# Kernel tuning notes

Hardware: AMD Instinct MI355X
Metric: run time of the kernel (lower is better)

## Reference

```python
import jax, jax.numpy as jnp
import numpy as np
from jax import lax

NUM_CLASSES = 2
MAX_DET = 300
SCORE_THR = 0.001
IOU_THR = 0.7
EPS = 1e-7


def _probiou_pairwise(b):
    # b: [M,5] = (cx, cy, w, h, angle). Gaussian-based rotated-box IoU (ProbIoU).
    cx, cy, w, h, t = (b[:, i] for i in range(5))
    ct, st = jnp.cos(t), jnp.sin(t)
    w2, h2 = w * w / 12.0, h * h / 12.0
    a = w2 * ct * ct + h2 * st * st
    bb = w2 * st * st + h2 * ct * ct
    c = (w2 - h2) * ct * st
    x1, y1, a1, b1, c1 = cx[:, None], cy[:, None], a[:, None], bb[:, None], c[:, None]
    x2, y2, a2, b2, c2 = cx[None, :], cy[None, :], a[None, :], bb[None, :], c[None, :]
    denom = (a1 + a2) * (b1 + b2) - (c1 + c2) ** 2 + EPS
    t1 = 0.25 * ((a1 + a2) * (y1 - y2) ** 2 + (b1 + b2) * (x1 - x2) ** 2) / denom
    t2 = 0.5 * ((c1 + c2) * (x2 - x1) * (y1 - y2)) / denom
    det1 = jnp.maximum(a1 * b1 - c1 * c1, 0.0)
    det2 = jnp.maximum(a2 * b2 - c2 * c2, 0.0)
    t3 = 0.5 * jnp.log(denom / (4.0 * jnp.sqrt(det1 * det2) + EPS) + EPS)
    bd = jnp.clip(t1 + t2 + t3, EPS, 100.0)
    hd = jnp.sqrt(1.0 - jnp.exp(-bd) + EPS)
    return 1.0 - hd


def _nms_single(boxes5, scores):
    # boxes5: [N,5], scores: [N,C] -> class-aware greedy rotated NMS
    N, C = scores.shape
    M = N * C
    cand_boxes = jnp.broadcast_to(boxes5[:, None, :], (N, C, 5)).reshape(M, 5)
    cand_scores = scores.reshape(M)
    cand_labels = jnp.broadcast_to(jnp.arange(C, dtype=jnp.int32)[None, :], (N, C)).reshape(M)
    order = jnp.argsort(-cand_scores)
    b, s, l = cand_boxes[order], cand_scores[order], cand_labels[order]
    iou = _probiou_pairwise(b)                          # [M,M]
    same = l[:, None] == l[None, :]
    sup = (iou > IOU_THR) & same
    idx = jnp.arange(M)
    valid = s > SCORE_THR

    def body(i, keep):
        row = sup[i] & (idx > i) & keep[i]
        return keep & ~row

    keep = lax.fori_loop(0, M, body, valid)
    sel = jnp.where(keep, s, -1.0)
    top = jnp.argsort(-sel)[:MAX_DET]
    ok = sel[top] > 0.0
    out_boxes = jnp.where(ok[:, None], b[top], 0.0)     # [MAX_DET,5]
    out_scores = jnp.where(ok, s[top], 0.0)             # [MAX_DET]
    out_labels = jnp.where(ok, l[top], 0)               # [MAX_DET] int32
    n_valid = jnp.minimum(jnp.sum(keep), MAX_DET).astype(jnp.int32)
    return out_boxes, out_scores, out_labels, n_valid


def _forward(x, conv_w, conv_b, bbox_w, bbox_b, cls_w, cls_b, ang_w, ang_b):
    B = x.shape[0]
    f = lax.conv_general_dilated(x, conv_w, (1, 1), 'SAME',
                                 dimension_numbers=('NCHW', 'OIHW', 'NCHW'))
    f = jax.nn.relu(f + conv_b[None, :, None, None])
    f = lax.reduce_window(f, -jnp.inf, lax.max, (1, 1, 2, 2), (1, 1, 2, 2), 'VALID')
    Hp, Wp = f.shape[2], f.shape[3]
    hw = Hp * Wp
    # 1x1-conv heads (materialized like the original), then spatial mean
    boxes = (jnp.einsum('bchw,oc->bohw', f, bbox_w) + bbox_b[None, :, None, None]
             ).reshape(B, MAX_DET, 4, hw).mean(-1)
    logits = (jnp.einsum('bchw,oc->bohw', f, cls_w) + cls_b[None, :, None, None]
              ).reshape(B, MAX_DET, NUM_CLASSES, hw).mean(-1)
    scores = jax.nn.softmax(logits, axis=2)
    angles = (jnp.einsum('bchw,oc->bohw', f, ang_w) + ang_b[None, :, None, None]
              ).reshape(B, MAX_DET, 1, hw).mean(-1)
    boxes5 = jnp.concatenate([boxes, angles], axis=-1)  # [B,300,5]
    return jax.vmap(_nms_single)(boxes5, scores)


def setup_inputs() -> dict:
    key = jax.random.key(0)
    ks = jax.random.split(key, 10)
    B, H, W = 4, 256, 256
    s = 0.1
    return {
        'x': jax.random.normal(ks[0], (B, 3, H, W), jnp.float32),
        'conv_w': jax.random.normal(ks[1], (16, 3, 3, 3), jnp.float32) * s,
        'conv_b': jax.random.normal(ks[2], (16,), jnp.float32) * s,
        'bbox_w': jax.random.normal(ks[3], (4 * MAX_DET, 16), jnp.float32) * s,
        'bbox_b': jax.random.normal(ks[4], (4 * MAX_DET,), jnp.float32) * s,
        'cls_w': jax.random.normal(ks[5], (NUM_CLASSES * MAX_DET, 16), jnp.float32) * s,
        'cls_b': jax.random.normal(ks[6], (NUM_CLASSES * MAX_DET,), jnp.float32) * s,
        'ang_w': jax.random.normal(ks[7], (MAX_DET, 16), jnp.float32) * s,
        'ang_b': jax.random.normal(ks[8], (MAX_DET,), jnp.float32) * s,
    }


def reference(x, conv_w, conv_b, bbox_w, bbox_b, cls_w, cls_b, ang_w, ang_b):
    return _forward(x, conv_w, conv_b, bbox_w, bbox_b, cls_w, cls_b, ang_w, ang_b)
```

## Files before the change

kernel.cpp:

```cpp
#include <hip/hip_runtime.h>
#include <hip/hip_bf16.h>

#define MAX_DET 300
#define NCAND 600
#define NPAD 640
#define SCORE_THR 1e-3f
#define IOU_THR 0.7f
#define EPSF 1e-7f

typedef float float4u __attribute__((ext_vector_type(4), aligned(4)));


static __device__ inline unsigned long long readlane64(unsigned long long v, int l) {
  unsigned int lo = (unsigned int)v;
  unsigned int hi = (unsigned int)(v >> 32);
  unsigned int slo = (unsigned int)__builtin_amdgcn_readlane((int)lo, l);
  unsigned int shi = (unsigned int)__builtin_amdgcn_readlane((int)hi, l);
  return ((unsigned long long)shi << 32) | (unsigned long long)slo;
}

__global__ __launch_bounds__(256) void k_conv_pool(
    const float* __restrict__ x, const float* __restrict__ cw,
    const float* __restrict__ cb, float* __restrict__ partial) {
  const int blk = blockIdx.x;
  const int chunk = blk & 7;
  const int oc = (blk >> 3) & 15;
  const int b = blk >> 7;
  const int tid = threadIdx.x;

  float w[27];
#pragma unroll
  for (int i = 0; i < 27; ++i) w[i] = cw[oc * 27 + i];
  const float bias = cb[oc];
  const float* xb = x + b * 3 * 65536;

  const int strip = chunk * 256 + tid;
  const int py = strip >> 4;
  const int x0 = (strip & 15) * 8;

  float cc0[8], cc1[8], cc2[8], cc3[8];
#pragma unroll
  for (int i = 0; i < 8; ++i) { cc0[i] = 0.f; cc1[i] = 0.f; cc2[i] = 0.f; cc3[i] = 0.f; }

#pragma unroll
  for (int ic = 0; ic < 3; ++ic) {
    const float* xc = xb + ic * 65536;
    const float* wc = w + ic * 9;
#pragma unroll
    for (int r = 0; r < 4; ++r) {
      const int y = 2 * py - 1 + r;
      if (y < 0 || y > 255) continue;
      const float* xr = xc + y * 256;
      float buf[20];
#pragma unroll
      for (int k = 0; k < 5; ++k) {
        const int c0 = 2 * x0 - 1 + 4 * k;
        if (c0 >= 0 && c0 + 3 <= 255) {
          const float4u v = *reinterpret_cast<const float4u*>(xr + c0);
          buf[4 * k + 0] = v.x; buf[4 * k + 1] = v.y;
          buf[4 * k + 2] = v.z; buf[4 * k + 3] = v.w;
        } else {
#pragma unroll
          for (int j = 0; j < 4; ++j) {
            const int c = c0 + j;
            buf[4 * k + j] = (c >= 0 && c <= 255) ? xr[c] : 0.f;
          }
        }
      }
#pragma unroll
      for (int i = 0; i < 8; ++i) {
        const float b0 = buf[2 * i], b1 = buf[2 * i + 1],
                    b2 = buf[2 * i + 2], b3 = buf[2 * i + 3];
        if (r <= 2) {
          const float w0 = wc[r * 3], w1 = wc[r * 3 + 1], w2 = wc[r * 3 + 2];
          cc0[i] += b0 * w0 + b1 * w1 + b2 * w2;
          cc1[i] += b1 * w0 + b2 * w1 + b3 * w2;
        }
        if (r >= 1) {
          const float w0 = wc[(r - 1) * 3], w1 = wc[(r - 1) * 3 + 1],
                      w2 = wc[(r - 1) * 3 + 2];
          cc2[i] += b0 * w0 + b1 * w1 + b2 * w2;
          cc3[i] += b1 * w0 + b2 * w1 + b3 * w2;
        }
      }
    }
  }

  float acc = 0.f;
#pragma unroll
  for (int i = 0; i < 8; ++i) {
    const float m = fmaxf(fmaxf(cc0[i], cc1[i]), fmaxf(cc2[i], cc3[i]));
    acc += fmaxf(m + bias, 0.f);
  }

  __shared__ float red[256];
  red[tid] = acc;
  __syncthreads();
  for (int s = 128; s > 0; s >>= 1) {
    if (tid < s) red[tid] += red[tid + s];
    __syncthreads();
  }
  if (tid == 0) partial[blk] = red[0];
}

__global__ __launch_bounds__(256) void k_prep(
    const float* __restrict__ partial,
    const float* __restrict__ bw, const float* __restrict__ bb,
    const float* __restrict__ cwm, const float* __restrict__ cbb,
    const float* __restrict__ aw, const float* __restrict__ ab,
    float* __restrict__ boxes5, float* __restrict__ sparams,
    int* __restrict__ order_g) {
  const int b = blockIdx.x;
  const int tid = threadIdx.x;
  const int wid = tid >> 6, lane = tid & 63;

  __shared__ float fm[16];
  __shared__ float sc[NPAD];
  __shared__ float sbox[MAX_DET * 5];
  __shared__ int order[NCAND];

  if (tid < 16) {
    float s = 0.f;
    for (int k = 0; k < 8; ++k) s += partial[(b * 16 + tid) * 8 + k];
    fm[tid] = s * (1.0f / 16384.0f);
  }
  for (int m = NCAND + tid; m < NPAD; m += 256) sc[m] = -1e30f;
  __syncthreads();

  float f[16];
#pragma unroll
  for (int k = 0; k < 16; ++k) f[k] = fm[k];

  for (int det = tid; det < MAX_DET; det += 256) {
    float out5[5];
#pragma unroll
    for (int j = 0; j < 4; ++j) {
      const int o = det * 4 + j;
      float acc = bb[o];
#pragma unroll
      for (int k = 0; k < 16; ++k) acc += bw[o * 16 + k] * f[k];
      out5[j] = acc;
    }
    {
      float acc = ab[det];
#pragma unroll
      for (int k = 0; k < 16; ++k) acc += aw[det * 16 + k] * f[k];
      out5[4] = acc;
    }
    float l0, l1;
    {
      const int o = det * 2;
      float a0 = cbb[o], a1 = cbb[o + 1];
#pragma unroll
      for (int k = 0; k < 16; ++k) {
        a0 += cwm[o * 16 + k] * f[k];
        a1 += cwm[(o + 1) * 16 + k] * f[k];
      }
      l0 = a0; l1 = a1;
    }
    const float mx = fmaxf(l0, l1);
    const float e0 = expf(l0 - mx), e1 = expf(l1 - mx);
    const float inv = 1.f / (e0 + e1);

#pragma unroll
    for (int j = 0; j < 5; ++j) {
      sbox[det * 5 + j] = out5[j];
      boxes5[(b * MAX_DET + det) * 5 + j] = out5[j];
    }
    sc[det * 2 + 0] = e0 * inv;
    sc[det * 2 + 1] = e1 * inv;
  }
  __syncthreads();

  float sreg[10];
#pragma unroll
  for (int k = 0; k < 10; ++k) sreg[k] = sc[k * 64 + lane];

#pragma unroll
  for (int w = 0; w < 10; ++w) {
#pragma unroll
    for (int t = 0; t < 16; ++t) {
      const int i = w * 64 + wid + 4 * t;
      if (i < NCAND) {
        float si;
        switch (w) {
          case 0: si = __shfl(sreg[0], i & 63); break;
          case 1: si = __shfl(sreg[1], i & 63); break;
          case 2: si = __shfl(sreg[2], i & 63); break;
          case 3: si = __shfl(sreg[3], i & 63); break;
          case 4: si = __shfl(sreg[4], i & 63); break;
          case 5: si = __shfl(sreg[5], i & 63); break;
          case 6: si = __shfl(sreg[6], i & 63); break;
          case 7: si = __shfl(sreg[7], i & 63); break;
          case 8: si = __shfl(sreg[8], i & 63); break;
          default: si = __shfl(sreg[9], i & 63); break;
        }
        int r = 0;
#pragma unroll
        for (int k = 0; k < 10; ++k) {
          const int j = k * 64 + lane;
          const bool c = (sreg[k] > si) || (sreg[k] == si && j < i);
          r += (int)__popcll(__ballot(c));
        }
        if (lane == 0) order[r] = i;
      }
    }
  }
  __syncthreads();

  float* P = sparams + b * 7 * NPAD;
  for (int r = tid; r < NCAND; r += 256) {
    const int i = order[r];
    order_g[b * NPAD + r] = i;
    const float* bp = sbox + (i >> 1) * 5;
    const float cx = bp[0], cy = bp[1], w = bp[2], h = bp[3], t = bp[4];
    const float ct = cosf(t), st = sinf(t);
    const float w2 = w * w * (1.f / 12.f), h2 = h * h * (1.f / 12.f);
    const float a = w2 * ct * ct + h2 * st * st;
    const float bb2 = w2 * st * st + h2 * ct * ct;
    const float c = (w2 - h2) * ct * st;
    P[0 * NPAD + r] = cx;
    P[1 * NPAD + r] = cy;
    P[2 * NPAD + r] = a;
    P[3 * NPAD + r] = bb2;
    P[4 * NPAD + r] = c;
    P[5 * NPAD + r] = fmaxf(a * bb2 - c * c, 0.f);
    P[6 * NPAD + r] = sc[i];
  }
}

__global__ __launch_bounds__(256) void k_mask(
    const float* __restrict__ sparams, const int* __restrict__ order_g,
    unsigned long long* __restrict__ mask) {
  const int wid = threadIdx.x >> 6, lane = threadIdx.x & 63;
  const int g = blockIdx.x * 4 + wid;
  const int b = g / NCAND, i = g % NCAND;

  const float* P = sparams + b * 7 * NPAD;
  const int* og = order_g + b * NPAD;
  const float x1 = P[i], y1 = P[NPAD + i], a1 = P[2 * NPAD + i],
              b1 = P[3 * NPAD + i], c1 = P[4 * NPAD + i], d1 = P[5 * NPAD + i];
  const int li = og[i] & 1;

#pragma unroll
  for (int w = 0; w < 10; ++w) {
    const int j = w * 64 + lane;
    const int jc = j < NCAND ? j : NCAND - 1;
    const float x2 = P[jc], y2 = P[NPAD + jc], a2 = P[2 * NPAD + jc],
                b2 = P[3 * NPAD + jc], c2 = P[4 * NPAD + jc],
                d2 = P[5 * NPAD + jc];
    const float as = a1 + a2, bs = b1 + b2, cs = c1 + c2;
    const float dxx = x2 - x1, dyy = y1 - y2;
    const float denom = as * bs - cs * cs + EPSF;
    const float rden = 1.f / denom;
    const float t1v = 0.25f * (as * dyy * dyy + bs * dxx * dxx) * rden;
    const float t2v = 0.5f * (cs * dxx * dyy) * rden;
    const float t3v = 0.5f * logf(denom / (4.f * sqrtf(d1 * d2) + EPSF) + EPSF);
    float bd = t1v + t2v + t3v;
    bd = fminf(fmaxf(bd, EPSF), 100.f);
    const float hd = sqrtf(1.f - expf(-bd) + EPSF);
    const bool cond = (j > i) && (j < NCAND) && ((og[jc] & 1) == li) &&
                      ((1.f - hd) > IOU_THR);
    const unsigned long long mw = __ballot(cond);
    if (lane == 0) mask[(b * NCAND + i) * 10 + w] = mw;
  }
}

__global__ __launch_bounds__(256) void k_scan(
    const float* __restrict__ boxes5, const float* __restrict__ sparams,
    const int* __restrict__ order_g, const unsigned long long* __restrict__ mask,
    float* __restrict__ out) {
  const int b = blockIdx.x;
  const int tid = threadIdx.x;
  const int wid = tid >> 6, lane = tid & 63;

  __shared__ unsigned long long m[NCAND * 10];
  __shared__ float ssc[NCAND];
  __shared__ unsigned long long keepw[10];
  __shared__ unsigned long long validbm[10];
  __shared__ unsigned long long nzbm[10];

  const unsigned long long* mg = mask + b * NCAND * 10;
  for (int k = tid; k < NCAND * 10; k += 256) m[k] = mg[k];
  const float* P = sparams + b * 7 * NPAD;
  for (int k = tid; k < NCAND; k += 256) ssc[k] = P[6 * NPAD + k];
  __syncthreads();

#pragma unroll
  for (int it = 0; it < 3; ++it) {
    const int g = wid + 4 * it;
    if (g < 10) {
      const int r = g * 64 + lane;
      bool valid = false;
      unsigned long long nzr = 0ULL;
      if (r < NCAND) {
        valid = ssc[r] > SCORE_THR;
        for (int k = 0; k < 10; ++k) nzr |= m[r * 10 + k];
      }
      const unsigned long long vb = __ballot(valid);
      const unsigned long long nb = __ballot(nzr != 0ULL);
      if (lane == 0) { validbm[g] = vb; nzbm[g] = nb; }
    }
  }
  __syncthreads();

  if (tid < 64) {
    unsigned long long keep = (lane < 10) ? validbm[lane] : 0ULL;
    const unsigned long long nzv = (lane < 10) ? nzbm[lane] : 0ULL;
#pragma unroll
    for (int w = 0; w < 10; ++w) {
      unsigned long long nzs = readlane64(nzv, w);
      unsigned long long ks = readlane64(keep, w);
      while (nzs) {
        const int bit = __builtin_ctzll(nzs);
        nzs &= nzs - 1ULL;
        if ((ks >> bit) & 1ULL) {
          const int i = w * 64 + bit;
          unsigned long long row = 0ULL;
          if (lane < 10) row = m[i * 10 + lane];
          keep &= ~row;
          ks &= ~readlane64(row, w);
        }
      }
    }
    if (lane < 10) keepw[lane] = keep;
  }
  __syncthreads();

  for (int k = tid; k < MAX_DET * 5; k += 256) out[b * MAX_DET * 5 + k] = 0.f;
  for (int k = tid; k < MAX_DET; k += 256) {
    out[6000 + b * MAX_DET + k] = 0.f;
    out[7200 + b * MAX_DET + k] = 0.f;
  }
  __syncthreads();

  const int* og = order_g + b * NPAD;
  for (int r = tid; r < NCAND; r += 256) {
    const int w = r >> 6, bitp = r & 63;
    if ((keepw[w] >> bitp) & 1ULL) {
      int pos = 0;
      for (int ww = 0; ww < w; ++ww) pos += __popcll(keepw[ww]);
      pos += __popcll(keepw[w] & ((1ULL << bitp) - 1ULL));
      if (pos < MAX_DET) {
        const int i = og[r];
        const float* bp = boxes5 + (b * MAX_DET + (i >> 1)) * 5;
        float* ob = out + (b * MAX_DET + pos) * 5;
        ob[0] = bp[0]; ob[1] = bp[1]; ob[2] = bp[2]; ob[3] = bp[3]; ob[4] = bp[4];
        out[6000 + b * MAX_DET + pos] = ssc[r];
        out[7200 + b * MAX_DET + pos] = (float)(i & 1);
      }
    }
  }
  if (tid == 0) {
    int total = 0;
    for (int ww = 0; ww < 10; ++ww) total += __popcll(keepw[ww]);
    if (total > MAX_DET) total = MAX_DET;
    out[8400 + b] = (float)total;
  }
}

extern "C" void kernel_launch(void* const* d_in, const int* in_sizes, int n_in,
                              void* d_out, int out_size, void* d_ws, size_t ws_size,
                              hipStream_t stream) {
  const float* x      = (const float*)d_in[0];
  const float* conv_w = (const float*)d_in[1];
  const float* conv_b = (const float*)d_in[2];
  const float* bbox_w = (const float*)d_in[3];
  const float* bbox_b = (const float*)d_in[4];
  const float* cls_w  = (const float*)d_in[5];
  const float* cls_b  = (const float*)d_in[6];
  const float* ang_w  = (const float*)d_in[7];
  const float* ang_b  = (const float*)d_in[8];
  float* out = (float*)d_out;
  float* ws = (float*)d_ws;

  float* partial = ws;
  float* boxes5  = ws + 1024;
  float* sparams = ws + 8720;
  int*   order_g = (int*)(ws + 26640);
  unsigned long long* mask = (unsigned long long*)(ws + 29200);

  k_conv_pool<<<512, 256, 0, stream>>>(x, conv_w, conv_b, partial);
  k_prep<<<4, 256, 0, stream>>>(partial, bbox_w, bbox_b, cls_w, cls_b,
                                ang_w, ang_b, boxes5, sparams, order_g);
  k_mask<<<600, 256, 0, stream>>>(sparams, order_g, mask);
  k_scan<<<4, 256, 0, stream>>>(boxes5, sparams, order_g, mask, out);
}
```

Before: 66.21 us.

## Fuse mask and scan kernels via last-block atomic counter; simplify prep

Merges the IoU mask kernel and the greedy NMS scan kernel into one launch. An atomic per-image counter elects the last finishing block, which then runs the scan, so one kernel launch and its inter-kernel gap go away. A hipMemsetAsync is added to reset the counters, and the last block per image adds a serial tail after its own mask work. The prep kernel also splits the linear heads into per-output loops with vectorized weight loads, and the rank computation is simplified to read scores from LDS instead of the switch-based shuffles.

```diff
diff --git a/kernel.cpp b/kernel.cpp
--- a/kernel.cpp
+++ b/kernel.cpp
@@ -131,44 +131,49 @@
 #pragma unroll
   for (int k = 0; k < 16; ++k) f[k] = fm[k];
 
-  for (int det = tid; det < MAX_DET; det += 256) {
-    float out5[5];
-#pragma unroll
-    for (int j = 0; j < 4; ++j) {
-      const int o = det * 4 + j;
-      float acc = bb[o];
-#pragma unroll
-      for (int k = 0; k < 16; ++k) acc += bw[o * 16 + k] * f[k];
-      out5[j] = acc;
-    }
-    {
-      float acc = ab[det];
-#pragma unroll
-      for (int k = 0; k < 16; ++k) acc += aw[det * 16 + k] * f[k];
-      out5[4] = acc;
-    }
-    float l0, l1;
-    {
-      const int o = det * 2;
-      float a0 = cbb[o], a1 = cbb[o + 1];
-#pragma unroll
-      for (int k = 0; k < 16; ++k) {
-        a0 += cwm[o * 16 + k] * f[k];
-        a1 += cwm[(o + 1) * 16 + k] * f[k];
-      }
-      l0 = a0; l1 = a1;
-    }
-    const float mx = fmaxf(l0, l1);
-    const float e0 = expf(l0 - mx), e1 = expf(l1 - mx);
+  for (int o = tid; o < 4 * MAX_DET; o += 256) {
+    const float4u* wp = reinterpret_cast<const float4u*>(bw + o * 16);
+    const float4u v0 = wp[0], v1 = wp[1], v2 = wp[2], v3 = wp[3];
+    float wrow[16] = {v0.x, v0.y, v0.z, v0.w, v1.x, v1.y, v1.z, v1.w,
+                      v2.x, v2.y, v2.z, v2.w, v3.x, v3.y, v3.z, v3.w};
+    float acc = bb[o];
+#pragma unroll
+    for (int k = 0; k < 16; ++k) acc += wrow[k] * f[k];
+    const int d = o >> 2, j = o & 3;
+    sbox[d * 5 + j] = acc;
+    boxes5[(b * MAX_DET + d) * 5 + j] = acc;
+  }
+  for (int o = tid; o < MAX_DET; o += 256) {
+    const float4u* wp = reinterpret_cast<const float4u*>(aw + o * 16);
+    const float4u v0 = wp[0], v1 = wp[1], v2 = wp[2], v3 = wp[3];
+    float wrow[16] = {v0.x, v0.y, v0.z, v0.w, v1.x, v1.y, v1.z, v1.w,
+                      v2.x, v2.y, v2.z, v2.w, v3.x, v3.y, v3.z, v3.w};
+    float acc = ab[o];
+#pragma unroll
+    for (int k = 0; k < 16; ++k) acc += wrow[k] * f[k];
+    sbox[o * 5 + 4] = acc;
+    boxes5[(b * MAX_DET + o) * 5 + 4] = acc;
+  }
+  for (int p = tid; p < MAX_DET; p += 256) {
+    const float4u* wp0 = reinterpret_cast<const float4u*>(cwm + (2 * p) * 16);
+    const float4u* wp1 = reinterpret_cast<const float4u*>(cwm + (2 * p + 1) * 16);
+    const float4u u0 = wp0[0], u1 = wp0[1], u2 = wp0[2], u3 = wp0[3];
+    const float4u t0 = wp1[0], t1 = wp1[1], t2 = wp1[2], t3 = wp1[3];
+    float w0r[16] = {u0.x, u0.y, u0.z, u0.w, u1.x, u1.y, u1.z, u1.w,
+                     u2.x, u2.y, u2.z, u2.w, u3.x, u3.y, u3.z, u3.w};
+    float w1r[16] = {t0.x, t0.y, t0.z, t0.w, t1.x, t1.y, t1.z, t1.w,
+                     t2.x, t2.y, t2.z, t2.w, t3.x, t3.y, t3.z, t3.w};
+    float a0 = cbb[2 * p], a1 = cbb[2 * p + 1];
+#pragma unroll
+    for (int k = 0; k < 16; ++k) {
+      a0 += w0r[k] * f[k];
+      a1 += w1r[k] * f[k];
+    }
+    const float mx = fmaxf(a0, a1);
+    const float e0 = expf(a0 - mx), e1 = expf(a1 - mx);
     const float inv = 1.f / (e0 + e1);
-
-#pragma unroll
-    for (int j = 0; j < 5; ++j) {
-      sbox[det * 5 + j] = out5[j];
-      boxes5[(b * MAX_DET + det) * 5 + j] = out5[j];
-    }
-    sc[det * 2 + 0] = e0 * inv;
-    sc[det * 2 + 1] = e1 * inv;
+    sc[p * 2 + 0] = e0 * inv;
+    sc[p * 2 + 1] = e1 * inv;
   }
   __syncthreads();
 
@@ -176,35 +181,18 @@
 #pragma unroll
   for (int k = 0; k < 10; ++k) sreg[k] = sc[k * 64 + lane];
 
-#pragma unroll
-  for (int w = 0; w < 10; ++w) {
-#pragma unroll
-    for (int t = 0; t < 16; ++t) {
-      const int i = w * 64 + wid + 4 * t;
-      if (i < NCAND) {
-        float si;
-        switch (w) {
-          case 0: si = __shfl(sreg[0], i & 63); break;
-          case 1: si = __shfl(sreg[1], i & 63); break;
-          case 2: si = __shfl(sreg[2], i & 63); break;
-          case 3: si = __shfl(sreg[3], i & 63); break;
-          case 4: si = __shfl(sreg[4], i & 63); break;
-          case 5: si = __shfl(sreg[5], i & 63); break;
-          case 6: si = __shfl(sreg[6], i & 63); break;
-          case 7: si = __shfl(sreg[7], i & 63); break;
-          case 8: si = __shfl(sreg[8], i & 63); break;
-          default: si = __shfl(sreg[9], i & 63); break;
-        }
-        int r = 0;
-#pragma unroll
-        for (int k = 0; k < 10; ++k) {
-          const int j = k * 64 + lane;
-          const bool c = (sreg[k] > si) || (sreg[k] == si && j < i);
-          r += (int)__popcll(__ballot(c));
-        }
-        if (lane == 0) order[r] = i;
-      }
-    }
+#pragma unroll 4
+  for (int t = 0; t < 150; ++t) {
+    const int i = t * 4 + wid;
+    const float si = sc[i];
+    int r = 0;
+#pragma unroll
+    for (int k = 0; k < 10; ++k) {
+      const int j = k * 64 + lane;
+      const bool c = (sreg[k] > si) || (sreg[k] == si && j < i);
+      r += (int)__popcll(__ballot(c));
+    }
+    if (lane == 0) order[r] = i;
   }
   __syncthreads();
 
@@ -229,50 +217,56 @@
   }
 }
 
-__global__ __launch_bounds__(256) void k_mask(
-    const float* __restrict__ sparams, const int* __restrict__ order_g,
-    unsigned long long* __restrict__ mask) {
-  const int wid = threadIdx.x >> 6, lane = threadIdx.x & 63;
-  const int g = blockIdx.x * 4 + wid;
-  const int b = g / NCAND, i = g % NCAND;
+__global__ __launch_bounds__(256) void k_masknms(
+    const float* __restrict__ boxes5, const float* __restrict__ sparams,
+    const int* __restrict__ order_g, unsigned long long* __restrict__ mask,
+    int* __restrict__ cnt, float* __restrict__ out) {
+  const int blk = blockIdx.x;
+  const int b = blk / 150;
+  const int tid = threadIdx.x;
+  const int wid = tid >> 6, lane = tid & 63;
+  const int i = (blk % 150) * 4 + wid;
 
   const float* P = sparams + b * 7 * NPAD;
   const int* og = order_g + b * NPAD;
-  const float x1 = P[i], y1 = P[NPAD + i], a1 = P[2 * NPAD + i],
-              b1 = P[3 * NPAD + i], c1 = P[4 * NPAD + i], d1 = P[5 * NPAD + i];
-  const int li = og[i] & 1;
-
-#pragma unroll
-  for (int w = 0; w < 10; ++w) {
-    const int j = w * 64 + lane;
-    const int jc = j < NCAND ? j : NCAND - 1;
-    const float x2 = P[jc], y2 = P[NPAD + jc], a2 = P[2 * NPAD + jc],
-                b2 = P[3 * NPAD + jc], c2 = P[4 * NPAD + jc],
-                d2 = P[5 * NPAD + jc];
-    const float as = a1 + a2, bs = b1 + b2, cs = c1 + c2;
-    const float dxx = x2 - x1, dyy = y1 - y2;
-    const float denom = as * bs - cs * cs + EPSF;
-    const float rden = 1.f / denom;
-    const float t1v = 0.25f * (as * dyy * dyy + bs * dxx * dxx) * rden;
-    const float t2v = 0.5f * (cs * dxx * dyy) * rden;
-    const float t3v = 0.5f * logf(denom / (4.f * sqrtf(d1 * d2) + EPSF) + EPSF);
-    float bd = t1v + t2v + t3v;
-    bd = fminf(fmaxf(bd, EPSF), 100.f);
-    const float hd = sqrtf(1.f - expf(-bd) + EPSF);
-    const bool cond = (j > i) && (j < NCAND) && ((og[jc] & 1) == li) &&
-                      ((1.f - hd) > IOU_THR);
-    const unsigned long long mw = __ballot(cond);
-    if (lane == 0) mask[(b * NCAND + i) * 10 + w] = mw;
-  }
-}
-
-__global__ __launch_bounds__(256) void k_scan(
-    const float* __restrict__ boxes5, const float* __restrict__ sparams,
-    const int* __restrict__ order_g, const unsigned long long* __restrict__ mask,
-    float* __restrict__ out) {
-  const int b = blockIdx.x;
-  const int tid = threadIdx.x;
-  const int wid = tid >> 6, lane = tid & 63;
+  {
+    const float x1 = P[i], y1 = P[NPAD + i], a1 = P[2 * NPAD + i],
+                b1 = P[3 * NPAD + i], c1 = P[4 * NPAD + i], d1 = P[5 * NPAD + i];
+    const int li = og[i] & 1;
+#pragma unroll
+    for (int w = 0; w < 10; ++w) {
+      const int j = w * 64 + lane;
+      const int jc = j < NCAND ? j : NCAND - 1;
+      const float x2 = P[jc], y2 = P[NPAD + jc], a2 = P[2 * NPAD + jc],
+                  b2 = P[3 * NPAD + jc], c2 = P[4 * NPAD + jc],
+                  d2 = P[5 * NPAD + jc];
+      const float as = a1 + a2, bs = b1 + b2, cs = c1 + c2;
+      const float dxx = x2 - x1, dyy = y1 - y2;
+      const float denom = as * bs - cs * cs + EPSF;
+      const float rden = 1.f / denom;
+      const float t1v = 0.25f * (as * dyy * dyy + bs * dxx * dxx) * rden;
+      const float t2v = 0.5f * (cs * dxx * dyy) * rden;
+      const float t3v = 0.5f * logf(denom / (4.f * sqrtf(d1 * d2) + EPSF) + EPSF);
+      float bd = t1v + t2v + t3v;
+      bd = fminf(fmaxf(bd, EPSF), 100.f);
+      const float hd = sqrtf(1.f - expf(-bd) + EPSF);
+      const bool cond = (j > i) && (j < NCAND) && ((og[jc] & 1) == li) &&
+                        ((1.f - hd) > IOU_THR);
+      const unsigned long long mw = __ballot(cond);
+      if (lane == 0) mask[(b * NCAND + i) * 10 + w] = mw;
+    }
+  }
+
+  __shared__ int lastflag;
+  __threadfence();
+  __syncthreads();
+  if (tid == 0) {
+    const int old = atomicAdd(&cnt[b], 1);
+    lastflag = (old == 149);
+  }
+  __syncthreads();
+  if (!lastflag) return;
+  __threadfence();
 
   __shared__ unsigned long long m[NCAND * 10];
   __shared__ float ssc[NCAND];
@@ -282,7 +276,6 @@
 
   const unsigned long long* mg = mask + b * NCAND * 10;
   for (int k = tid; k < NCAND * 10; k += 256) m[k] = mg[k];
-  const float* P = sparams + b * 7 * NPAD;
   for (int k = tid; k < NCAND; k += 256) ssc[k] = P[6 * NPAD + k];
   __syncthreads();
 
@@ -315,9 +308,9 @@
         const int bit = __builtin_ctzll(nzs);
         nzs &= nzs - 1ULL;
         if ((ks >> bit) & 1ULL) {
-          const int i = w * 64 + bit;
+          const int ii = w * 64 + bit;
           unsigned long long row = 0ULL;
-          if (lane < 10) row = m[i * 10 + lane];
+          if (lane < 10) row = m[ii * 10 + lane];
           keep &= ~row;
           ks &= ~readlane64(row, w);
         }
@@ -334,7 +327,6 @@
   }
   __syncthreads();
 
-  const int* og = order_g + b * NPAD;
   for (int r = tid; r < NCAND; r += 256) {
     const int w = r >> 6, bitp = r & 63;
     if ((keepw[w] >> bitp) & 1ULL) {
@@ -342,12 +334,12 @@
       for (int ww = 0; ww < w; ++ww) pos += __popcll(keepw[ww]);
       pos += __popcll(keepw[w] & ((1ULL << bitp) - 1ULL));
       if (pos < MAX_DET) {
-        const int i = og[r];
-        const float* bp = boxes5 + (b * MAX_DET + (i >> 1)) * 5;
+        const int idx = og[r];
+        const float* bp = boxes5 + (b * MAX_DET + (idx >> 1)) * 5;
         float* ob = out + (b * MAX_DET + pos) * 5;
         ob[0] = bp[0]; ob[1] = bp[1]; ob[2] = bp[2]; ob[3] = bp[3]; ob[4] = bp[4];
         out[6000 + b * MAX_DET + pos] = ssc[r];
-        out[7200 + b * MAX_DET + pos] = (float)(i & 1);
+        out[7200 + b * MAX_DET + pos] = (float)(idx & 1);
       }
     }
   }
@@ -379,10 +371,11 @@
   float* sparams = ws + 8720;
   int*   order_g = (int*)(ws + 26640);
   unsigned long long* mask = (unsigned long long*)(ws + 29200);
-
+  int*   cnt     = (int*)(ws + 77200);
+
+  hipMemsetAsync(cnt, 0, 4 * sizeof(int), stream);
   k_conv_pool<<<512, 256, 0, stream>>>(x, conv_w, conv_b, partial);
   k_prep<<<4, 256, 0, stream>>>(partial, bbox_w, bbox_b, cls_w, cls_b,
                                 ang_w, ang_b, boxes5, sparams, order_g);
-  k_mask<<<600, 256, 0, stream>>>(sparams, order_g, mask);
-  k_scan<<<4, 256, 0, stream>>>(boxes5, sparams, order_g, mask, out);
-}
+  k_masknms<<<600, 256, 0, stream>>>(boxes5, sparams, order_g, mask, cnt, out);
+}
```

After: 111.0 us. 67.6% more time.
